# Kernel tuning notes

Measured on AMD Instinct MI355X. Metric: run time of the kernel, lower is better.

Reference implementation:

```python
import jax, jax.numpy as jnp
import numpy as np
from jax import lax

B, T, H, THETA_DIM = 64, 2048, 256, 5
L1, L2, OUT = 256, 256, 1


def _p(key, shape, fan_in):
    return jax.random.normal(key, shape, dtype=jnp.float32) / np.sqrt(fan_in)


def setup_inputs() -> dict:
    key = jax.random.key(0)
    ks = jax.random.split(key, 16)
    inp = {
        "x": jax.random.normal(ks[0], (B, T), dtype=jnp.float32),
        "theta": jax.random.normal(ks[1], (B, THETA_DIM), dtype=jnp.float32),
        # LSTM layer 0 (input dim 1): gate order [i, f, g, o]
        "Wx0": _p(ks[2], (1, 4 * H), 1),
        "Wh0": _p(ks[3], (H, 4 * H), H),
        "b0": jnp.zeros((4 * H,), dtype=jnp.float32),
        # LSTM layer 1 (input dim H)
        "Wx1": _p(ks[4], (H, 4 * H), H),
        "Wh1": _p(ks[5], (H, 4 * H), H),
        "b1": jnp.zeros((4 * H,), dtype=jnp.float32),
        # theta projector Dense(H)
        "Wtp": _p(ks[6], (THETA_DIM, H), THETA_DIM),
        "btp": jnp.zeros((H,), dtype=jnp.float32),
        # MLP head: concat(H + H) -> 256 -> 256 -> 1
        "Wl1": _p(ks[7], (2 * H, L1), 2 * H),
        "bl1": jnp.zeros((L1,), dtype=jnp.float32),
        "Wl2": _p(ks[8], (L1, L2), L1),
        "bl2": jnp.zeros((L2,), dtype=jnp.float32),
        "Wo": _p(ks[9], (L2, OUT), L2),
        "bo": jnp.zeros((OUT,), dtype=jnp.float32),
    }
    return inp


def _lstm_layer(x_seq, Wx, Wh, b):
    # x_seq: [B, T, D]. Precompute input-to-gate GEMM once (big, batched),
    # leaving only the small recurrent matmul inside the scan.
    xg = jnp.einsum('btd,dg->btg', x_seq, Wx) + b  # [B, T, 4H]
    bsz = x_seq.shape[0]
    h = Wh.shape[0]
    c0 = jnp.zeros((bsz, h), dtype=x_seq.dtype)
    h0 = jnp.zeros((bsz, h), dtype=x_seq.dtype)

    def step(carry, xg_t):
        c, hh = carry
        gates = xg_t + hh @ Wh  # [B, 4H]
        i, f, g, o = jnp.split(gates, 4, axis=-1)
        c = jax.nn.sigmoid(f) * c + jax.nn.sigmoid(i) * jnp.tanh(g)
        hh = jax.nn.sigmoid(o) * jnp.tanh(c)
        return (c, hh), hh

    _, hs = lax.scan(step, (c0, h0), jnp.swapaxes(xg, 0, 1))  # hs: [T, B, H]
    return jnp.swapaxes(hs, 0, 1)  # [B, T, H]


def reference(x, theta, Wx0, Wh0, b0, Wx1, Wh1, b1, Wtp, btp,
              Wl1, bl1, Wl2, bl2, Wo, bo):
    h = x[:, :, None]  # [B, T, 1] (module expands 2-D input)
    h = _lstm_layer(h, Wx0, Wh0, b0)
    h = _lstm_layer(h, Wx1, Wh1, b1)
    h = jnp.mean(h, axis=1)  # mean_aggregation=True -> [B, H]
    tproj = theta @ Wtp + btp  # [B, H]
    z = jnp.concatenate([h, tproj], axis=-1)  # [B, 2H]
    z = jax.nn.elu(z @ Wl1 + bl1)
    z = jax.nn.elu(z @ Wl2 + bl2)
    return z @ Wo + bo  # [B, 1]
```

## Files before the change

kernel.cpp:

```cpp
#include <hip/hip_runtime.h>
#include <hip/hip_bf16.h>


#define BB 64
#define TT 2048
#define HH 256
#define D0 16
#define D1 4

typedef short s16x8 __attribute__((ext_vector_type(8)));
typedef float f32x4 __attribute__((ext_vector_type(4)));

__device__ inline unsigned short f2bf(float f) {
  unsigned u = __float_as_uint(f);
  u += 0x7fff + ((u >> 16) & 1);
  return (unsigned short)(u >> 16);
}
__device__ inline float sigm(float x) { return 1.f / (1.f + __expf(-x)); }
__device__ inline float tanh_f(float x) { return 1.f - 2.f / (__expf(2.f * x) + 1.f); }

__device__ inline unsigned long long ld64(const unsigned int* p) {
  return __hip_atomic_load((const unsigned long long*)p, __ATOMIC_RELAXED,
                           __HIP_MEMORY_SCOPE_AGENT);
}
__device__ inline void st32(unsigned int* p, unsigned int v) {
  __hip_atomic_store(p, v, __ATOMIC_RELAXED, __HIP_MEMORY_SCOPE_AGENT);
}
__device__ inline void st32i(int* p, int v) {
  __hip_atomic_store(p, v, __ATOMIC_RELAXED, __HIP_MEMORY_SCOPE_AGENT);
}
__device__ inline int ld32i(const int* p) {
  return __hip_atomic_load(p, __ATOMIC_RELAXED, __HIP_MEMORY_SCOPE_AGENT);
}
__device__ inline void wg_bar() {
  asm volatile("s_waitcnt lgkmcnt(0)" ::: "memory");
  __builtin_amdgcn_sched_barrier(0);
  __builtin_amdgcn_s_barrier();
  __builtin_amdgcn_sched_barrier(0);
}

#define MFMA(a, b, c) __builtin_amdgcn_mfma_f32_16x16x32_bf16((a), (b), (c), 0, 0, 0)

__global__ void xt_kernel(const float* __restrict__ x, float* __restrict__ xT) {
  int i = blockIdx.x * 256 + threadIdx.x;
  int b = i & 63, t = i >> 6;
  xT[(size_t)t * BB + b] = x[(size_t)b * TT + t];
}

__global__ __launch_bounds__(512, 1)
void lstm_kernel(const float* __restrict__ Wx0, const float* __restrict__ Wh0,
                 const float* __restrict__ b0v,
                 const float* __restrict__ Wx1, const float* __restrict__ Wh1,
                 const float* __restrict__ b1v,
                 const float* __restrict__ xT,
                 unsigned int* __restrict__ seqring,
                 unsigned int* __restrict__ h1ring,
                 float* __restrict__ hmean, int* prog)
{
  __shared__ __align__(16) char Ab [8192];
  __shared__ __align__(16) char Ab1[8192];
  __shared__ float gbuf[16][4][66];

  const int tid  = threadIdx.x;
  const int lane = tid & 63;
  const int w    = tid >> 6;
  const int u16  = lane & 15;
  const int kgrp = lane >> 4;
  const int arow = lane & 15;
  const int bid  = blockIdx.x;

  if (bid < 8) {
    const int g = bid >> 1, ho = bid & 1, po = 1 - ho;
    const int U = ho * 128 + w * 16 + u16;
    s16x8 bw[32];
#pragma unroll
    for (int n = 0; n < 4; ++n)
#pragma unroll
      for (int ph = 0; ph < 2; ++ph)
#pragma unroll
        for (int i = 0; i < 4; ++i) {
          const int ks = (ph == 0 ? ho : po) * 4 + i;
          const int col = n * 256 + U;
#pragma unroll
          for (int j = 0; j < 8; ++j)
            bw[n * 8 + ph * 4 + i][j] =
                (short)f2bf(Wh0[(size_t)(ks * 32 + kgrp * 8 + j) * 1024 + col]);
        }
    float bE[4], xE[4];
#pragma unroll
    for (int n = 0; n < 4; ++n) { bE[n] = b0v[n * 256 + U]; xE[n] = Wx0[n * 256 + U]; }

    unsigned int* sr = seqring + (size_t)g * D0 * 4096;
    const int srow = tid >> 5, spc = (tid & 31) * 4;
    float cL[4] = {0.f, 0.f, 0.f, 0.f};
    unsigned long long pq0 = 0, pq1 = 0;

    for (int t = 0; t < TT; ++t) {
      if ((t & 7) == 0 && t >= 16 && tid < 4)
        while (ld32i(&prog[(g * 4 + tid) * 16]) < t - 8) __builtin_amdgcn_s_sleep(8);
      wg_bar();

      f32x4 acc[4] = {{0,0,0,0},{0,0,0,0},{0,0,0,0},{0,0,0,0}};
      if (t > 0) {
        s16x8 ao[4];
#pragma unroll
        for (int i = 0; i < 4; ++i) {
          const int ks = ho * 4 + i;
          ao[i] = *(const s16x8*)(Ab + ((arow * 512 + (ks * 32 + kgrp * 8) * 2) ^ ((arow & 7) << 4)));
        }
#pragma unroll
        for (int i = 0; i < 4; ++i)
#pragma unroll
          for (int n = 0; n < 4; ++n) acc[n] = MFMA(ao[i], bw[n * 8 + i], acc[n]);
        const unsigned int* sb = sr + ((t - 1) & (D0 - 1)) * 4096 + srow * 256 + po * 128 + spc;
        const unsigned int tg = (unsigned int)t;
        unsigned long long q0 = pq0, q1 = pq1;
        for (;;) {
          const bool ok = (((q0 >> 16) & 0xFFFFu) == tg) & ((unsigned)(q0 >> 48) == tg) &
                          (((q1 >> 16) & 0xFFFFu) == tg) & ((unsigned)(q1 >> 48) == tg);
          if (__all(ok)) break;
          __builtin_amdgcn_s_sleep(1);
          q0 = ld64(sb); q1 = ld64(sb + 2);
        }
        const unsigned int lo = (unsigned)(q0 & 0xFFFF) | (((unsigned)(q0 >> 32) & 0xFFFF) << 16);
        const unsigned int hi = (unsigned)(q1 & 0xFFFF) | (((unsigned)(q1 >> 32) & 0xFFFF) << 16);
        *(uint2*)(Ab + ((srow * 512 + (po * 128 + spc) * 2) ^ ((srow & 7) << 4))) = (uint2){lo, hi};
      }
      wg_bar();
      if (t > 0) {
        s16x8 ap[4];
#pragma unroll
        for (int i = 0; i < 4; ++i) {
          const int ks = po * 4 + i;
          ap[i] = *(const s16x8*)(Ab + ((arow * 512 + (ks * 32 + kgrp * 8) * 2) ^ ((arow & 7) << 4)));
        }
#pragma unroll
        for (int i = 0; i < 4; ++i)
#pragma unroll
          for (int n = 0; n < 4; ++n) acc[n] = MFMA(ap[i], bw[n * 8 + 4 + i], acc[n]);
      }
      float xr[4];
#pragma unroll
      for (int r = 0; r < 4; ++r) xr[r] = xT[(size_t)t * BB + g * 16 + kgrp * 4 + r];
      const unsigned int tagw = (unsigned)(t + 1) << 16;
#pragma unroll
      for (int r = 0; r < 4; ++r) {
        const int row = kgrp * 4 + r;
        const float gi = acc[0][r] + bE[0] + xr[r] * xE[0];
        const float gf = acc[1][r] + bE[1] + xr[r] * xE[1];
        const float gg = acc[2][r] + bE[2] + xr[r] * xE[2];
        const float go = acc[3][r] + bE[3] + xr[r] * xE[3];
        cL[r] = sigm(gf) * cL[r] + sigm(gi) * tanh_f(gg);
        const float hv = sigm(go) * tanh_f(cL[r]);
        const unsigned short hb = f2bf(hv);
        st32(sr + (t & (D0 - 1)) * 4096 + row * 256 + U, tagw | hb);
        *(unsigned short*)(Ab + ((row * 512 + U * 2) ^ ((row & 7) << 4))) = hb;
      }
      {
        const unsigned int* sb = sr + (t & (D0 - 1)) * 4096 + srow * 256 + po * 128 + spc;
        pq0 = ld64(sb); pq1 = ld64(sb + 2);
      }
    }
  } else {
    const int idx = bid - 8, g = idx >> 2, q = idx & 3;
    const int gp = w >> 2;
    const int uo = (w & 3) * 16;
    const int ub = q * 64;
    s16x8 bw[2][16];
#pragma unroll
    for (int nt = 0; nt < 2; ++nt)
#pragma unroll
      for (int ks = 0; ks < 16; ++ks) {
        const int col = (2 * gp + nt) * 256 + ub + uo + u16;
#pragma unroll
        for (int j = 0; j < 8; ++j) {
          const int k = (ks & 7) * 32 + kgrp * 8 + j;
          bw[nt][ks][j] = (short)f2bf((ks < 8) ? Wx1[(size_t)k * 1024 + col]
                                               : Wh1[(size_t)k * 1024 + col]);
        }
      }
    const int eur = tid >> 5, eu2 = (tid & 31) * 2;
    float bE[4][2];
#pragma unroll
    for (int ga = 0; ga < 4; ++ga)
#pragma unroll
      for (int uu = 0; uu < 2; ++uu)
        bE[ga][uu] = b1v[ga * 256 + ub + eu2 + uu];

    unsigned int* sr = seqring + (size_t)g * D0 * 4096;
    unsigned int* hr = h1ring  + (size_t)g * D1 * 4096;
    const int srow = tid >> 5, sc8 = (tid & 31) * 8;
    float cL[2] = {0.f, 0.f}, hs[2] = {0.f, 0.f};
    unsigned long long qh0[4], qh1[4];

    {
      const unsigned int* sb = sr + srow * 256 + sc8;
#pragma unroll
      for (int i = 0; i < 4; ++i) qh0[i] = ld64(sb + i * 2);
    }

    for (int t = 0; t < TT; ++t) {
      if ((t & 3) == 3 && tid == 0) st32i(&prog[(g * 4 + q) * 16], t);
      {
        const unsigned int* sb = sr + (t & (D0 - 1)) * 4096 + srow * 256 + sc8;
        const unsigned int tg = (unsigned int)(t + 1);
        for (;;) {
          bool ok = true;
#pragma unroll
          for (int i = 0; i < 4; ++i)
            ok &= (((qh0[i] >> 16) & 0xFFFFu) == tg) & ((unsigned)(qh0[i] >> 48) == tg);
          if (__all(ok)) break;
          __builtin_amdgcn_s_sleep(1);
#pragma unroll
          for (int i = 0; i < 4; ++i) qh0[i] = ld64(sb + i * 2);
        }
        unsigned int wv[4];
#pragma unroll
        for (int i = 0; i < 4; ++i)
          wv[i] = (unsigned)(qh0[i] & 0xFFFF) | (((unsigned)(qh0[i] >> 32) & 0xFFFF) << 16);
        *(uint4*)(Ab + ((srow * 512 + sc8 * 2) ^ ((srow & 7) << 4))) =
            (uint4){wv[0], wv[1], wv[2], wv[3]};
      }
      wg_bar();
      f32x4 acc0 = {0,0,0,0}, acc1 = {0,0,0,0};
      {
        s16x8 a[8];
#pragma unroll
        for (int ks = 0; ks < 8; ++ks)
          a[ks] = *(const s16x8*)(Ab + ((arow * 512 + (ks * 32 + kgrp * 8) * 2) ^ ((arow & 7) << 4)));
#pragma unroll
        for (int ks = 0; ks < 8; ++ks) {
          acc0 = MFMA(a[ks], bw[0][ks], acc0);
          acc1 = MFMA(a[ks], bw[1][ks], acc1);
        }
      }
      if (t > 0) {
        const unsigned int* sb = hr + ((t - 1) & (D1 - 1)) * 4096 + srow * 256 + sc8;
        const unsigned int tg = (unsigned int)t;
        for (;;) {
          bool ok = true;
#pragma unroll
          for (int i = 0; i < 4; ++i)
            ok &= (((qh1[i] >> 16) & 0xFFFFu) == tg) & ((unsigned)(qh1[i] >> 48) == tg);
          if (__all(ok)) break;
          __builtin_amdgcn_s_sleep(1);
#pragma unroll
          for (int i = 0; i < 4; ++i) qh1[i] = ld64(sb + i * 2);
        }
        unsigned int wv[4];
#pragma unroll
        for (int i = 0; i < 4; ++i)
          wv[i] = (unsigned)(qh1[i] & 0xFFFF) | (((unsigned)(qh1[i] >> 32) & 0xFFFF) << 16);
        *(uint4*)(Ab1 + ((srow * 512 + sc8 * 2) ^ ((srow & 7) << 4))) =
            (uint4){wv[0], wv[1], wv[2], wv[3]};
      }
      wg_bar();
      if (t > 0) {
        s16x8 a[8];
#pragma unroll
        for (int kk = 0; kk < 8; ++kk)
          a[kk] = *(const s16x8*)(Ab1 + ((arow * 512 + (kk * 32 + kgrp * 8) * 2) ^ ((arow & 7) << 4)));
#pragma unroll
        for (int kk = 0; kk < 8; ++kk) {
          acc0 = MFMA(a[kk], bw[0][8 + kk], acc0);
          acc1 = MFMA(a[kk], bw[1][8 + kk], acc1);
        }
      }
#pragma unroll
      for (int r = 0; r < 4; ++r) {
        gbuf[kgrp * 4 + r][2 * gp + 0][uo + u16] = acc0[r];
        gbuf[kgrp * 4 + r][2 * gp + 1][uo + u16] = acc1[r];
      }
      wg_bar();

      unsigned short hb[2];
#pragma unroll
      for (int uu = 0; uu < 2; ++uu) {
        const int u = eu2 + uu;
        const float gi = gbuf[eur][0][u] + bE[0][uu];
        const float gf = gbuf[eur][1][u] + bE[1][uu];
        const float gg = gbuf[eur][2][u] + bE[2][uu];
        const float go = gbuf[eur][3][u] + bE[3][uu];
        cL[uu] = sigm(gf) * cL[uu] + sigm(gi) * tanh_f(gg);
        const float hv = sigm(go) * tanh_f(cL[uu]);
        hs[uu] += hv;
        hb[uu] = f2bf(hv);
      }
      const unsigned int tagw = (unsigned)(t + 1) << 16;
      st32(hr + (t & (D1 - 1)) * 4096 + eur * 256 + ub + eu2,     tagw | hb[0]);
      st32(hr + (t & (D1 - 1)) * 4096 + eur * 256 + ub + eu2 + 1, tagw | hb[1]);
      {
        const unsigned int* sb = sr + ((t + 1) & (D0 - 1)) * 4096 + srow * 256 + sc8;
#pragma unroll
        for (int i = 0; i < 4; ++i) qh0[i] = ld64(sb + i * 2);
        const unsigned int* hb2 = hr + (t & (D1 - 1)) * 4096 + srow * 256 + sc8;
#pragma unroll
        for (int i = 0; i < 4; ++i) qh1[i] = ld64(hb2 + i * 2);
      }
    }
#pragma unroll
    for (int uu = 0; uu < 2; ++uu)
      hmean[(size_t)(g * 16 + eur) * HH + ub + eu2 + uu] = hs[uu] * (1.f / TT);
  }
}

__global__ __launch_bounds__(256)
void mlp_kernel(const float* __restrict__ theta, const float* __restrict__ Wtp,
                const float* __restrict__ btp, const float* __restrict__ Wl1,
                const float* __restrict__ bl1, const float* __restrict__ Wl2,
                const float* __restrict__ bl2, const float* __restrict__ Wo,
                const float* __restrict__ bo, const float* __restrict__ hmean,
                float* __restrict__ out)
{
  const int b = blockIdx.x;
  const int j = threadIdx.x;
  __shared__ float z[2 * HH];
  __shared__ float z1s[HH];
  __shared__ float red[256];

  float tp = btp[j];
#pragma unroll
  for (int d = 0; d < 5; ++d) tp += theta[b * 5 + d] * Wtp[d * HH + j];
  z[j] = hmean[(size_t)b * HH + j];
  z[HH + j] = tp;
  __syncthreads();

  float a1 = bl1[j];
  for (int k = 0; k < 2 * HH; ++k) a1 += z[k] * Wl1[(size_t)k * 256 + j];
  a1 = (a1 > 0.f) ? a1 : (__expf(a1) - 1.f);
  z1s[j] = a1;
  __syncthreads();

  float a2 = bl2[j];
  for (int k = 0; k < HH; ++k) a2 += z1s[k] * Wl2[(size_t)k * 256 + j];
  a2 = (a2 > 0.f) ? a2 : (__expf(a2) - 1.f);
  red[j] = a2 * Wo[j];
  __syncthreads();
  for (int s = 128; s > 0; s >>= 1) {
    if (j < s) red[j] += red[j + s];
    __syncthreads();
  }
  if (j == 0) out[b] = red[0] + bo[0];
}

extern "C" void kernel_launch(void* const* d_in, const int* in_sizes, int n_in,
                              void* d_out, int out_size, void* d_ws, size_t ws_size,
                              hipStream_t stream) {
  const float* x    = (const float*)d_in[0];
  const float* theta= (const float*)d_in[1];
  const float* Wx0  = (const float*)d_in[2];
  const float* Wh0  = (const float*)d_in[3];
  const float* b0   = (const float*)d_in[4];
  const float* Wx1  = (const float*)d_in[5];
  const float* Wh1  = (const float*)d_in[6];
  const float* b1   = (const float*)d_in[7];
  const float* Wtp  = (const float*)d_in[8];
  const float* btp  = (const float*)d_in[9];
  const float* Wl1  = (const float*)d_in[10];
  const float* bl1  = (const float*)d_in[11];
  const float* Wl2  = (const float*)d_in[12];
  const float* bl2  = (const float*)d_in[13];
  const float* Wo   = (const float*)d_in[14];
  const float* bo   = (const float*)d_in[15];

  char* ws = (char*)d_ws;
  int* prog             = (int*)ws;
  unsigned int* seqring = (unsigned int*)(ws + 8192);
  unsigned int* h1ring  = (unsigned int*)(ws + 8192 + 1048576);
  float* hmean          = (float*)(ws + 8192 + 1048576 + 262144);
  float* xT             = (float*)(ws + 8192 + 1048576 + 262144 + 65536);
  const size_t WS_NEED = 8192ull + 1048576 + 262144 + 65536 + 524288;
  if (ws_size < WS_NEED) return;

  hipMemsetAsync(d_ws, 0, 8192 + 1048576 + 262144, stream);

  xt_kernel<<<dim3((BB * TT) / 256), dim3(256), 0, stream>>>(x, xT);
  lstm_kernel<<<dim3(24), dim3(512), 0, stream>>>(
      Wx0, Wh0, b0, Wx1, Wh1, b1, xT, seqring, h1ring, hmean, prog);
  mlp_kernel<<<dim3(BB), dim3(256), 0, stream>>>(
      theta, Wtp, btp, Wl1, bl1, Wl2, bl2, Wo, bo, hmean, (float*)d_out);
}
```

Baseline: 6.187 ms.

## Remap layer-1 gate columns so cell update uses shuffles instead of LDS barrier

Layer-1 workgroups now assign MFMA output columns so that the four gates of a hidden unit sit in lanes 4 apart. The cell update then gathers them with cross-lane xor shuffles instead of writing to a shared gate buffer and waiting on an extra workgroup barrier. The ring-buffer polling loads in both layers are moved to the start of each step, and the x load is hoisted earlier, so their latency overlaps with the MFMA work. In exchange, every lane computes redundant activations and only a quarter of the lanes store results.

```diff
diff --git a/kernel.cpp b/kernel.cpp
--- a/kernel.cpp
+++ b/kernel.cpp
@@ -59,7 +59,6 @@
 {
   __shared__ __align__(16) char Ab [8192];
   __shared__ __align__(16) char Ab1[8192];
-  __shared__ float gbuf[16][4][66];
 
   const int tid  = threadIdx.x;
   const int lane = tid & 63;
@@ -93,13 +92,19 @@
     unsigned int* sr = seqring + (size_t)g * D0 * 4096;
     const int srow = tid >> 5, spc = (tid & 31) * 4;
     float cL[4] = {0.f, 0.f, 0.f, 0.f};
-    unsigned long long pq0 = 0, pq1 = 0;
 
     for (int t = 0; t < TT; ++t) {
       if ((t & 7) == 0 && t >= 16 && tid < 4)
         while (ld32i(&prog[(g * 4 + tid) * 16]) < t - 8) __builtin_amdgcn_s_sleep(8);
       wg_bar();
 
+      unsigned long long q0 = 0, q1 = 0;
+      const unsigned int* sb = sr + ((t - 1) & (D0 - 1)) * 4096 + srow * 256 + po * 128 + spc;
+      if (t > 0) { q0 = ld64(sb); q1 = ld64(sb + 2); }
+      float xr[4];
+#pragma unroll
+      for (int r = 0; r < 4; ++r) xr[r] = xT[(size_t)t * BB + g * 16 + kgrp * 4 + r];
+
       f32x4 acc[4] = {{0,0,0,0},{0,0,0,0},{0,0,0,0},{0,0,0,0}};
       if (t > 0) {
         s16x8 ao[4];
@@ -112,9 +117,7 @@
         for (int i = 0; i < 4; ++i)
 #pragma unroll
           for (int n = 0; n < 4; ++n) acc[n] = MFMA(ao[i], bw[n * 8 + i], acc[n]);
-        const unsigned int* sb = sr + ((t - 1) & (D0 - 1)) * 4096 + srow * 256 + po * 128 + spc;
         const unsigned int tg = (unsigned int)t;
-        unsigned long long q0 = pq0, q1 = pq1;
         for (;;) {
           const bool ok = (((q0 >> 16) & 0xFFFFu) == tg) & ((unsigned)(q0 >> 48) == tg) &
                           (((q1 >> 16) & 0xFFFFu) == tg) & ((unsigned)(q1 >> 48) == tg);
@@ -139,9 +142,6 @@
 #pragma unroll
           for (int n = 0; n < 4; ++n) acc[n] = MFMA(ap[i], bw[n * 8 + 4 + i], acc[n]);
       }
-      float xr[4];
-#pragma unroll
-      for (int r = 0; r < 4; ++r) xr[r] = xT[(size_t)t * BB + g * 16 + kgrp * 4 + r];
       const unsigned int tagw = (unsigned)(t + 1) << 16;
 #pragma unroll
       for (int r = 0; r < 4; ++r) {
@@ -156,22 +156,18 @@
         st32(sr + (t & (D0 - 1)) * 4096 + row * 256 + U, tagw | hb);
         *(unsigned short*)(Ab + ((row * 512 + U * 2) ^ ((row & 7) << 4))) = hb;
       }
-      {
-        const unsigned int* sb = sr + (t & (D0 - 1)) * 4096 + srow * 256 + po * 128 + spc;
-        pq0 = ld64(sb); pq1 = ld64(sb + 2);
-      }
     }
   } else {
     const int idx = bid - 8, g = idx >> 2, q = idx & 3;
-    const int gp = w >> 2;
-    const int uo = (w & 3) * 16;
-    const int ub = q * 64;
+    const int ub  = q * 64;
+    const int go_ = u16 >> 2;
+    const int lu  = u16 & 3;
     s16x8 bw[2][16];
 #pragma unroll
     for (int nt = 0; nt < 2; ++nt)
 #pragma unroll
       for (int ks = 0; ks < 16; ++ks) {
-        const int col = (2 * gp + nt) * 256 + ub + uo + u16;
+        const int col = go_ * 256 + ub + w * 8 + nt * 4 + lu;
 #pragma unroll
         for (int j = 0; j < 8; ++j) {
           const int k = (ks & 7) * 32 + kgrp * 8 + j;
@@ -179,18 +175,15 @@
                                                : Wh1[(size_t)k * 1024 + col]);
         }
       }
-    const int eur = tid >> 5, eu2 = (tid & 31) * 2;
-    float bE[4][2];
-#pragma unroll
-    for (int ga = 0; ga < 4; ++ga)
-#pragma unroll
-      for (int uu = 0; uu < 2; ++uu)
-        bE[ga][uu] = b1v[ga * 256 + ub + eu2 + uu];
+    float bE[2];
+#pragma unroll
+    for (int nt = 0; nt < 2; ++nt) bE[nt] = b1v[go_ * 256 + ub + w * 8 + nt * 4 + lu];
 
     unsigned int* sr = seqring + (size_t)g * D0 * 4096;
     unsigned int* hr = h1ring  + (size_t)g * D1 * 4096;
     const int srow = tid >> 5, sc8 = (tid & 31) * 8;
-    float cL[2] = {0.f, 0.f}, hs[2] = {0.f, 0.f};
+    float cL[2][4] = {{0,0,0,0},{0,0,0,0}};
+    float hs[2][4] = {{0,0,0,0},{0,0,0,0}};
     unsigned long long qh0[4], qh1[4];
 
     {
@@ -201,6 +194,11 @@
 
     for (int t = 0; t < TT; ++t) {
       if ((t & 3) == 3 && tid == 0) st32i(&prog[(g * 4 + q) * 16], t);
+      const unsigned int* sbh1 = hr + ((t - 1) & (D1 - 1)) * 4096 + srow * 256 + sc8;
+      if (t > 0) {
+#pragma unroll
+        for (int i = 0; i < 4; ++i) qh1[i] = ld64(sbh1 + i * 2);
+      }
       {
         const unsigned int* sb = sr + (t & (D0 - 1)) * 4096 + srow * 256 + sc8;
         const unsigned int tg = (unsigned int)(t + 1);
@@ -235,7 +233,6 @@
         }
       }
       if (t > 0) {
-        const unsigned int* sb = hr + ((t - 1) & (D1 - 1)) * 4096 + srow * 256 + sc8;
         const unsigned int tg = (unsigned int)t;
         for (;;) {
           bool ok = true;
@@ -245,7 +242,7 @@
           if (__all(ok)) break;
           __builtin_amdgcn_s_sleep(1);
 #pragma unroll
-          for (int i = 0; i < 4; ++i) qh1[i] = ld64(sb + i * 2);
+          for (int i = 0; i < 4; ++i) qh1[i] = ld64(sbh1 + i * 2);
         }
         unsigned int wv[4];
 #pragma unroll
@@ -266,41 +263,45 @@
           acc1 = MFMA(a[kk], bw[1][8 + kk], acc1);
         }
       }
-#pragma unroll
-      for (int r = 0; r < 4; ++r) {
-        gbuf[kgrp * 4 + r][2 * gp + 0][uo + u16] = acc0[r];
-        gbuf[kgrp * 4 + r][2 * gp + 1][uo + u16] = acc1[r];
-      }
-      wg_bar();
-
-      unsigned short hb[2];
-#pragma unroll
-      for (int uu = 0; uu < 2; ++uu) {
-        const int u = eu2 + uu;
-        const float gi = gbuf[eur][0][u] + bE[0][uu];
-        const float gf = gbuf[eur][1][u] + bE[1][uu];
-        const float gg = gbuf[eur][2][u] + bE[2][uu];
-        const float go = gbuf[eur][3][u] + bE[3][uu];
-        cL[uu] = sigm(gf) * cL[uu] + sigm(gi) * tanh_f(gg);
-        const float hv = sigm(go) * tanh_f(cL[uu]);
-        hs[uu] += hv;
-        hb[uu] = f2bf(hv);
-      }
       const unsigned int tagw = (unsigned)(t + 1) << 16;
-      st32(hr + (t & (D1 - 1)) * 4096 + eur * 256 + ub + eu2,     tagw | hb[0]);
-      st32(hr + (t & (D1 - 1)) * 4096 + eur * 256 + ub + eu2 + 1, tagw | hb[1]);
+      const bool b0 = go_ & 1, b1 = go_ & 2;
+#pragma unroll
+      for (int nt = 0; nt < 2; ++nt) {
+        f32x4& an = (nt == 0) ? acc0 : acc1;
+#pragma unroll
+        for (int r = 0; r < 4; ++r) {
+          const float av = an[r] + bE[nt];
+          const float Bv = __shfl_xor(av, 4);
+          const float Cv = __shfl_xor(av, 8);
+          const float Dv = __shfl_xor(av, 12);
+          const float e0 = b0 ? Bv : av,  e1 = b0 ? av : Bv;
+          const float f0 = b0 ? Dv : Cv,  f1 = b0 ? Cv : Dv;
+          const float gi = (b1 ? f0 : e0);
+          const float gf = (b1 ? f1 : e1);
+          const float gg = (b1 ? e0 : f0);
+          const float go = (b1 ? e1 : f1);
+          cL[nt][r] = sigm(gf) * cL[nt][r] + sigm(gi) * tanh_f(gg);
+          const float hv = sigm(go) * tanh_f(cL[nt][r]);
+          hs[nt][r] += hv;
+          if (u16 < 4)
+            st32(hr + (t & (D1 - 1)) * 4096 + (kgrp * 4 + r) * 256 + ub + w * 8 + nt * 4 + lu,
+                 tagw | f2bf(hv));
+        }
+      }
       {
         const unsigned int* sb = sr + ((t + 1) & (D0 - 1)) * 4096 + srow * 256 + sc8;
 #pragma unroll
         for (int i = 0; i < 4; ++i) qh0[i] = ld64(sb + i * 2);
-        const unsigned int* hb2 = hr + (t & (D1 - 1)) * 4096 + srow * 256 + sc8;
-#pragma unroll
-        for (int i = 0; i < 4; ++i) qh1[i] = ld64(hb2 + i * 2);
       }
     }
-#pragma unroll
-    for (int uu = 0; uu < 2; ++uu)
-      hmean[(size_t)(g * 16 + eur) * HH + ub + eu2 + uu] = hs[uu] * (1.f / TT);
+    if (u16 < 4) {
+#pragma unroll
+      for (int nt = 0; nt < 2; ++nt)
+#pragma unroll
+        for (int r = 0; r < 4; ++r)
+          hmean[(size_t)(g * 16 + kgrp * 4 + r) * HH + ub + w * 8 + nt * 4 + lu] =
+              hs[nt][r] * (1.f / TT);
+    }
   }
 }
 
```

Result: slower. 12.62 ms (+104.0%).
